# Kernel optimization log

Measured on AMD Instinct MI355X. Metric: run time of the kernel, lower is better.

## Reference

```python
import jax, jax.numpy as jnp
import numpy as np

TAU0 = 0.5  # Concrete temperature (init kwarg tau0)
EPS = float(np.finfo(np.float32).eps)  # torch.finfo(float32).eps clamp


def _linear_params(key, fan_in, fan_out):
    # matches torch nn.Linear default init: U(-1/sqrt(fan_in), 1/sqrt(fan_in))
    bound = 1.0 / np.sqrt(fan_in)
    kw, kb = jax.random.split(key)
    W = jax.random.uniform(kw, (fan_in, fan_out), minval=-bound, maxval=bound, dtype=jnp.float32)
    b = jax.random.uniform(kb, (fan_out,), minval=-bound, maxval=bound, dtype=jnp.float32)
    return W, b


def setup_inputs() -> dict:
    key = jax.random.key(0)
    ks = jax.random.split(key, 6)
    B, D, K = 32768, 200, 10
    w1, b1 = _linear_params(ks[0], D, 100)    # dense1
    w2, b2 = _linear_params(ks[1], 100, 100)  # dense2
    wl, bl = _linear_params(ks[2], 100, D)    # logits
    wo, bo = _linear_params(ks[3], D, 2)      # output (requires D == 200)
    x = jax.random.normal(ks[4], (B, D), dtype=jnp.float32)
    uniform = jax.random.uniform(ks[5], (B, K, D), dtype=jnp.float32)
    return {"x": x, "uniform": uniform,
            "w1": w1, "b1": b1, "w2": w2, "b2": b2,
            "wl": wl, "bl": bl, "wo": wo, "bo": bo}


def reference(x, uniform, w1, b1, w2, b2, wl, bl, wo, bo):
    # selector MLP
    h = jax.nn.relu(x @ w1 + b1)            # (B, 100)
    h = jax.nn.relu(h @ w2 + b2)            # (B, 100)
    logits = h @ wl + bl                    # (B, D)
    # SampleConcrete (training path): gumbel-softmax over features, max over k samples
    u = jnp.clip(uniform, EPS, 1.0)         # (B, K, D)
    gumbel = -jnp.log(-jnp.log(u))
    noisy = (gumbel + logits[:, None, :]) / TAU0
    samples = jax.nn.softmax(noisy, axis=-1).max(axis=1)  # (B, D); repeat_count == 1
    xs = x * samples
    preds = jax.nn.softmax(xs @ wo + bo, axis=-1)          # (B, 2)
    # hsic(xs, preds) in the original is computed but discarded -> omitted
    return preds, samples
```

## Files before the change

kernel.cpp:

```cpp
#include <hip/hip_runtime.h>
#include <hip/hip_bf16.h>

__launch_bounds__(256)
__global__ void fused_mlp12(const float* __restrict__ x,
                            const float* __restrict__ w1, const float* __restrict__ b1,
                            const float* __restrict__ w2, const float* __restrict__ b2,
                            float* __restrict__ h2out) {
  constexpr int BM = 64, KC = 20, BMP = 68;
  __shared__ float At[KC * BMP];
  __shared__ float Ws[KC * 128];
  __shared__ float h1T[100 * BMP];

  const int t = threadIdx.x;
  const int tx = t & 31;
  const int ty = t >> 5;
  const int rowBase = blockIdx.x * BM;

  float acc[8][4];
#pragma unroll
  for (int i = 0; i < 8; i++)
#pragma unroll
    for (int j = 0; j < 4; j++) acc[i][j] = 0.0f;

  for (int kc = 0; kc < 200; kc += KC) {
#pragma unroll
    for (int i = t; i < BM * KC; i += 256) {
      int r = i / KC, k = i - r * KC;
      At[k * BMP + r] = x[(rowBase + r) * 200 + kc + k];
    }
#pragma unroll
    for (int i = t; i < KC * 128; i += 256) {
      int k = i >> 7, c = i & 127;
      Ws[i] = (c < 100) ? w1[(kc + k) * 100 + c] : 0.0f;
    }
    __syncthreads();
#pragma unroll
    for (int k = 0; k < KC; k++) {
      float a[8], b[4];
      *(float4*)&a[0] = *(const float4*)&At[k * BMP + ty * 8];
      *(float4*)&a[4] = *(const float4*)&At[k * BMP + ty * 8 + 4];
      *(float4*)&b[0] = *(const float4*)&Ws[k * 128 + tx * 4];
#pragma unroll
      for (int i = 0; i < 8; i++)
#pragma unroll
        for (int j = 0; j < 4; j++) acc[i][j] += a[i] * b[j];
    }
    __syncthreads();
  }

  if (tx < 25) {
#pragma unroll
    for (int i = 0; i < 8; i++) {
      const int r = ty * 8 + i;
#pragma unroll
      for (int j = 0; j < 4; j++) {
        const int c = tx * 4 + j;
        h1T[c * BMP + r] = fmaxf(acc[i][j] + b1[c], 0.0f);
      }
    }
  }
  __syncthreads();

#pragma unroll
  for (int i = 0; i < 8; i++)
#pragma unroll
    for (int j = 0; j < 4; j++) acc[i][j] = 0.0f;

  for (int kc = 0; kc < 100; kc += KC) {
#pragma unroll
    for (int i = t; i < KC * 128; i += 256) {
      int k = i >> 7, c = i & 127;
      Ws[i] = (c < 100) ? w2[(kc + k) * 100 + c] : 0.0f;
    }
    __syncthreads();
#pragma unroll
    for (int k = 0; k < KC; k++) {
      float a[8], b[4];
      *(float4*)&a[0] = *(const float4*)&h1T[(kc + k) * BMP + ty * 8];
      *(float4*)&a[4] = *(const float4*)&h1T[(kc + k) * BMP + ty * 8 + 4];
      *(float4*)&b[0] = *(const float4*)&Ws[k * 128 + tx * 4];
#pragma unroll
      for (int i = 0; i < 8; i++)
#pragma unroll
        for (int j = 0; j < 4; j++) acc[i][j] += a[i] * b[j];
    }
    __syncthreads();
  }

  if (tx < 25) {
#pragma unroll
    for (int i = 0; i < 8; i++) {
      const int r = rowBase + ty * 8 + i;
      float4 v;
      v.x = fmaxf(acc[i][0] + b2[tx * 4 + 0], 0.0f);
      v.y = fmaxf(acc[i][1] + b2[tx * 4 + 1], 0.0f);
      v.z = fmaxf(acc[i][2] + b2[tx * 4 + 2], 0.0f);
      v.w = fmaxf(acc[i][3] + b2[tx * 4 + 3], 0.0f);
      *(float4*)&h2out[r * 100 + tx * 4] = v;
    }
  }
}

__launch_bounds__(512, 4)
__global__ void fused_logits_concrete(const float* __restrict__ x,
                                      const float* __restrict__ uniform,
                                      const float* __restrict__ h2,
                                      const float* __restrict__ wl, const float* __restrict__ bl,
                                      const float* __restrict__ wo, const float* __restrict__ bo,
                                      float* __restrict__ out, int B) {
  constexpr int BM = 64, KC = 20, BMP = 68;
  constexpr float EPS = 1.1920929e-07f;
  __shared__ float At[KC * BMP];
  __shared__ float Ws[KC * 256];
  __shared__ float lg[BM * 200];

  const int t = threadIdx.x;
  const int rowBase = blockIdx.x * BM;

  {
    const int tx = t & 31;
    const int ty = t >> 5;
    float acc[4][8];
#pragma unroll
    for (int i = 0; i < 4; i++)
#pragma unroll
      for (int j = 0; j < 8; j++) acc[i][j] = 0.0f;

    for (int kc = 0; kc < 100; kc += KC) {
      for (int i = t; i < BM * KC; i += 512) {
        int r = i / KC, k = i - r * KC;
        At[k * BMP + r] = h2[(rowBase + r) * 100 + kc + k];
      }
#pragma unroll
      for (int i = t; i < KC * 256; i += 512) {
        int k = i >> 8, c = i & 255;
        Ws[i] = (c < 200) ? wl[(kc + k) * 200 + c] : 0.0f;
      }
      __syncthreads();
#pragma unroll
      for (int k = 0; k < KC; k++) {
        float a[4], b[8];
        *(float4*)&a[0] = *(const float4*)&At[k * BMP + ty * 4];
        *(float4*)&b[0] = *(const float4*)&Ws[k * 256 + tx * 8];
        *(float4*)&b[4] = *(const float4*)&Ws[k * 256 + tx * 8 + 4];
#pragma unroll
        for (int i = 0; i < 4; i++)
#pragma unroll
          for (int j = 0; j < 8; j++) acc[i][j] += a[i] * b[j];
      }
      __syncthreads();
    }

    if (tx < 25) {
#pragma unroll
      for (int i = 0; i < 4; i++) {
        const int r = ty * 4 + i;
        float4 v0, v1;
        v0.x = acc[i][0] + bl[tx * 8 + 0];
        v0.y = acc[i][1] + bl[tx * 8 + 1];
        v0.z = acc[i][2] + bl[tx * 8 + 2];
        v0.w = acc[i][3] + bl[tx * 8 + 3];
        v1.x = acc[i][4] + bl[tx * 8 + 4];
        v1.y = acc[i][5] + bl[tx * 8 + 5];
        v1.z = acc[i][6] + bl[tx * 8 + 6];
        v1.w = acc[i][7] + bl[tx * 8 + 7];
        *(float4*)&lg[r * 200 + tx * 8] = v0;
        *(float4*)&lg[r * 200 + tx * 8 + 4] = v1;
      }
    }
    __syncthreads();
  }

  const int lane = t & 63;
  const int wave = t >> 6;
  const int samplesBase = B * 2;

#pragma unroll 1
  for (int rr = 0; rr < 8; rr++) {
    const int r = wave * 8 + rr;
    const int b = rowBase + r;

    float lgv[4], xv[4], smax[4];
#pragma unroll
    for (int i = 0; i < 4; i++) {
      const int d = lane + 64 * i;
      const bool v = (d < 200);
      lgv[i] = v ? lg[r * 200 + d] : 0.0f;
      xv[i] = v ? x[(size_t)b * 200 + d] : 0.0f;
      smax[i] = 0.0f;
    }

    const float* __restrict__ u = uniform + (size_t)b * 2000;
    float uu[10][4];
#pragma unroll
    for (int k = 0; k < 10; k++)
#pragma unroll
      for (int i = 0; i < 4; i++) {
        const int d = lane + 64 * i;
        uu[k][i] = (d < 200) ? u[k * 200 + d] : 0.5f;
      }

#pragma unroll
    for (int k = 0; k < 10; k++) {
      float noisy[4];
      float mloc = -1e30f;
#pragma unroll
      for (int i = 0; i < 4; i++) {
        if (lane + 64 * i < 200) {
          float uc = fminf(fmaxf(uu[k][i], EPS), 1.0f);
          const float g = -__logf(-__logf(uc));
          noisy[i] = (g + lgv[i]) * 2.0f;
          mloc = fmaxf(mloc, noisy[i]);
        } else {
          noisy[i] = -1e30f;
        }
      }
#pragma unroll
      for (int off = 32; off > 0; off >>= 1)
        mloc = fmaxf(mloc, __shfl_xor(mloc, off, 64));

      float e[4], ssum = 0.0f;
#pragma unroll
      for (int i = 0; i < 4; i++) {
        e[i] = (lane + 64 * i < 200) ? __expf(noisy[i] - mloc) : 0.0f;
        ssum += e[i];
      }
#pragma unroll
      for (int off = 32; off > 0; off >>= 1)
        ssum += __shfl_xor(ssum, off, 64);

      const float inv = 1.0f / ssum;
#pragma unroll
      for (int i = 0; i < 4; i++) smax[i] = fmaxf(smax[i], e[i] * inv);
    }

    float p0 = 0.0f, p1 = 0.0f;
#pragma unroll
    for (int i = 0; i < 4; i++) {
      const int d = lane + 64 * i;
      if (d < 200) {
        const float s = smax[i];
        out[samplesBase + (size_t)b * 200 + d] = s;
        const float xs = xv[i] * s;
        p0 += xs * wo[d * 2 + 0];
        p1 += xs * wo[d * 2 + 1];
      }
    }
#pragma unroll
    for (int off = 32; off > 0; off >>= 1) {
      p0 += __shfl_xor(p0, off, 64);
      p1 += __shfl_xor(p1, off, 64);
    }
    if (lane == 0) {
      const float z0 = p0 + bo[0];
      const float z1 = p1 + bo[1];
      const float m = fmaxf(z0, z1);
      const float e0 = __expf(z0 - m);
      const float e1 = __expf(z1 - m);
      out[b * 2 + 0] = e0 / (e0 + e1);
      out[b * 2 + 1] = e1 / (e0 + e1);
    }
  }
}

extern "C" void kernel_launch(void* const* d_in, const int* in_sizes, int n_in,
                              void* d_out, int out_size, void* d_ws, size_t ws_size,
                              hipStream_t stream) {
  const float* x  = (const float*)d_in[0];
  const float* un = (const float*)d_in[1];
  const float* w1 = (const float*)d_in[2];
  const float* b1 = (const float*)d_in[3];
  const float* w2 = (const float*)d_in[4];
  const float* b2 = (const float*)d_in[5];
  const float* wl = (const float*)d_in[6];
  const float* bl = (const float*)d_in[7];
  const float* wo = (const float*)d_in[8];
  const float* bo = (const float*)d_in[9];
  float* out = (float*)d_out;

  const int B = in_sizes[0] / 200;
  float* h2 = (float*)d_ws;

  fused_mlp12<<<B / 64, 256, 0, stream>>>(x, w1, b1, w2, b2, h2);
  fused_logits_concrete<<<B / 64, 512, 0, stream>>>(x, un, h2, wl, bl, wo, bo, out, B);
}
```

Before: 565.7 us.

## Rewrite Gumbel-softmax algebraically and alias shared memory for higher occupancy

With temperature 0.5, exp(2*(g+logit)) equals exp(2*logit)/log(u)^2, so the per-sample inner loop now needs one log2 and one reciprocal per element. The row max is taken once over the logits rather than once per sample. The base-2 log scale cancels in the normalisation. The uniform samples are streamed with a two-deep register buffer instead of preloading all ten, and the logits tile now shares LDS with the GEMM staging buffers, so the launch bound can ask for 6 blocks per CU. This cuts transcendental work, one cross-lane reduction per sample and register/LDS pressure, at some risk to numerical behaviour for u near 1 and to the clamp semantics.

```diff
diff --git a/kernel.cpp b/kernel.cpp
--- a/kernel.cpp
+++ b/kernel.cpp
@@ -101,7 +101,7 @@
   }
 }
 
-__launch_bounds__(512, 4)
+__launch_bounds__(512, 6)
 __global__ void fused_logits_concrete(const float* __restrict__ x,
                                       const float* __restrict__ uniform,
                                       const float* __restrict__ h2,
@@ -110,9 +110,10 @@
                                       float* __restrict__ out, int B) {
   constexpr int BM = 64, KC = 20, BMP = 68;
   constexpr float EPS = 1.1920929e-07f;
-  __shared__ float At[KC * BMP];
-  __shared__ float Ws[KC * 256];
-  __shared__ float lg[BM * 200];
+  __shared__ float smem[BM * 200];
+  float* const At = smem;
+  float* const Ws = smem + KC * BMP;
+  float* const lg = smem;
 
   const int t = threadIdx.x;
   const int rowBase = blockIdx.x * BM;
@@ -173,65 +174,57 @@
 
   const int lane = t & 63;
   const int wave = t >> 6;
-  const int samplesBase = B * 2;
+  const size_t samplesBase = (size_t)B * 2;
 
 #pragma unroll 1
   for (int rr = 0; rr < 8; rr++) {
     const int r = wave * 8 + rr;
     const int b = rowBase + r;
-
-    float lgv[4], xv[4], smax[4];
+    const float* __restrict__ u = uniform + (size_t)b * 2000;
+
+    float lgv[4], xv[4];
+    bool vld[4];
 #pragma unroll
     for (int i = 0; i < 4; i++) {
       const int d = lane + 64 * i;
-      const bool v = (d < 200);
-      lgv[i] = v ? lg[r * 200 + d] : 0.0f;
-      xv[i] = v ? x[(size_t)b * 200 + d] : 0.0f;
-      smax[i] = 0.0f;
-    }
-
-    const float* __restrict__ u = uniform + (size_t)b * 2000;
-    float uu[10][4];
-#pragma unroll
-    for (int k = 0; k < 10; k++)
+      vld[i] = (d < 200);
+      lgv[i] = vld[i] ? lg[r * 200 + d] : -1e30f;
+      xv[i]  = vld[i] ? x[(size_t)b * 200 + d] : 0.0f;
+    }
+
+    float m = fmaxf(fmaxf(lgv[0], lgv[1]), fmaxf(lgv[2], lgv[3]));
+#pragma unroll
+    for (int off = 32; off > 0; off >>= 1) m = fmaxf(m, __shfl_xor(m, off, 64));
+
+    float el[4];
+#pragma unroll
+    for (int i = 0; i < 4; i++) el[i] = vld[i] ? __expf(2.0f * (lgv[i] - m)) : 0.0f;
+
+    float smax[4] = {0.0f, 0.0f, 0.0f, 0.0f};
+
+    float uc[2][4];
+#pragma unroll
+    for (int i = 0; i < 4; i++) uc[0][i] = vld[i] ? u[lane + 64 * i] : 0.5f;
+
+#pragma unroll
+    for (int k = 0; k < 10; k++) {
+      if (k < 9) {
+#pragma unroll
+        for (int i = 0; i < 4; i++)
+          uc[(k + 1) & 1][i] = vld[i] ? u[(k + 1) * 200 + lane + 64 * i] : 0.5f;
+      }
+      float s[4], ssum = 0.0f;
 #pragma unroll
       for (int i = 0; i < 4; i++) {
-        const int d = lane + 64 * i;
-        uu[k][i] = (d < 200) ? u[k * 200 + d] : 0.5f;
-      }
-
-#pragma unroll
-    for (int k = 0; k < 10; k++) {
-      float noisy[4];
-      float mloc = -1e30f;
-#pragma unroll
-      for (int i = 0; i < 4; i++) {
-        if (lane + 64 * i < 200) {
-          float uc = fminf(fmaxf(uu[k][i], EPS), 1.0f);
-          const float g = -__logf(-__logf(uc));
-          noisy[i] = (g + lgv[i]) * 2.0f;
-          mloc = fmaxf(mloc, noisy[i]);
-        } else {
-          noisy[i] = -1e30f;
-        }
-      }
-#pragma unroll
-      for (int off = 32; off > 0; off >>= 1)
-        mloc = fmaxf(mloc, __shfl_xor(mloc, off, 64));
-
-      float e[4], ssum = 0.0f;
-#pragma unroll
-      for (int i = 0; i < 4; i++) {
-        e[i] = (lane + 64 * i < 200) ? __expf(noisy[i] - mloc) : 0.0f;
-        ssum += e[i];
-      }
-#pragma unroll
-      for (int off = 32; off > 0; off >>= 1)
-        ssum += __shfl_xor(ssum, off, 64);
-
-      const float inv = 1.0f / ssum;
-#pragma unroll
-      for (int i = 0; i < 4; i++) smax[i] = fmaxf(smax[i], e[i] * inv);
+        const float q = __log2f(fmaxf(uc[k & 1][i], EPS));
+        s[i] = el[i] * __builtin_amdgcn_rcpf(q * q);
+        ssum += s[i];
+      }
+#pragma unroll
+      for (int off = 32; off > 0; off >>= 1) ssum += __shfl_xor(ssum, off, 64);
+      const float inv = __builtin_amdgcn_rcpf(ssum);
+#pragma unroll
+      for (int i = 0; i < 4; i++) smax[i] = fmaxf(smax[i], s[i] * inv);
     }
 
     float p0 = 0.0f, p1 = 0.0f;
@@ -254,9 +247,9 @@
     if (lane == 0) {
       const float z0 = p0 + bo[0];
       const float z1 = p1 + bo[1];
-      const float m = fmaxf(z0, z1);
-      const float e0 = __expf(z0 - m);
-      const float e1 = __expf(z1 - m);
+      const float mh = fmaxf(z0, z1);
+      const float e0 = __expf(z0 - mh);
+      const float e1 = __expf(z1 - mh);
       out[b * 2 + 0] = e0 / (e0 + e1);
       out[b * 2 + 1] = e1 / (e0 + e1);
     }
```

New measurement: 581.8 us. 2.9% more time.
